# Kernel optimization log

Hardware: AMD Instinct MI355X
Metric: run time of the kernel (lower is better)

## Reference

```python
import jax, jax.numpy as jnp
import numpy as np

N_NODES = 50000
N_EDGES = 262144
N_OCP = 32768
N_GRAPHS = 64
H = 128          # hidden_size
F_IN = 128       # node feature dim (== H for the stub GNN)
N_LABELS = 10


def _lin(key, fan_in, fan_out):
    return jax.random.normal(key, (fan_in, fan_out), jnp.float32) * (1.0 / float(np.sqrt(fan_in)))


def setup_inputs() -> dict:
    key = jax.random.key(0)
    ks = jax.random.split(key, 16)
    x = jax.random.normal(ks[0], (N_NODES, F_IN), jnp.float32)
    edge_index = jax.random.randint(ks[1], (2, N_EDGES), 0, N_NODES)
    batch_vec = jnp.sort(jax.random.randint(ks[2], (N_NODES,), 0, N_GRAPHS))
    y = jax.random.randint(ks[3], (N_GRAPHS,), 0, N_LABELS)
    params = {
        # stub GNN (get_node_reps): one GCN-style layer
        'W_self': _lin(ks[4], F_IN, H),
        'W_nbr': _lin(ks[5], F_IN, H),
        'b_gnn': jnp.zeros((H,), jnp.float32),
        # edge_action_rep_generator: Linear(2H,4H) ELU Linear(4H,2H) ELU Linear(2H,H)
        'Wr1': _lin(ks[6], 2 * H, 4 * H), 'br1': jnp.zeros((4 * H,), jnp.float32),
        'Wr2': _lin(ks[7], 4 * H, 2 * H), 'br2': jnp.zeros((2 * H,), jnp.float32),
        'Wr3': _lin(ks[8], 2 * H, H),     'br3': jnp.zeros((H,), jnp.float32),
        # edge_action_prob_generator: Linear(H,H) ELU Linear(H,num_labels)
        'Wp1': _lin(ks[9], H, H),         'bp1': jnp.zeros((H,), jnp.float32),
        'Wp2': _lin(ks[10], H, N_LABELS), 'bp2': jnp.zeros((N_LABELS,), jnp.float32),
    }
    return dict(x=x, edge_index=edge_index, batch_vec=batch_vec, y=y, n_ocp=N_OCP, **params)


def reference(x, edge_index, batch_vec, y, n_ocp,
              W_self, W_nbr, b_gnn,
              Wr1, br1, Wr2, br2, Wr3, br3,
              Wp1, bp1, Wp2, bp2):
    N = x.shape[0]
    G = y.shape[0]

    def get_node_reps(ei):
        # stub for self.model.get_node_reps: elu(x @ W_self + A @ (x @ W_nbr))
        msg = x[ei[0]] @ W_nbr                                   # [E', H]
        agg = jax.ops.segment_sum(msg, ei[1], num_segments=N)    # [N, H]
        return jax.nn.elu(x @ W_self + agg + b_gnn)

    ocp_edge_index = edge_index[:, :n_ocp]    # state == True edges
    ava_edge_index = edge_index[:, n_ocp:]    # state == False edges

    ava_node_reps = get_node_reps(edge_index) - get_node_reps(ocp_edge_index)  # [N, H]

    # gather per available edge + concat src/dst reps -> [E_ava, 2H]
    a = jnp.concatenate([ava_node_reps[ava_edge_index[0]],
                         ava_node_reps[ava_edge_index[1]]], axis=1)
    # edge_action_rep_generator
    a = jax.nn.elu(a @ Wr1 + br1)
    a = jax.nn.elu(a @ Wr2 + br2)
    a = a @ Wr3 + br3                                            # [E_ava, H]
    # edge_action_prob_generator
    h = jax.nn.elu(a @ Wp1 + bp1)
    logits = h @ Wp2 + bp2                                       # [E_ava, L]

    seg = batch_vec[ava_edge_index[0]]                           # graph id per ava edge
    y_edge = y[seg]                                              # target label per edge
    sel = jnp.take_along_axis(logits, y_edge[:, None], axis=1)[:, 0]  # gather(1, y)

    # segment-wise softmax over edges of each graph
    mx = jax.ops.segment_max(sel, seg, num_segments=G)
    ex = jnp.exp(sel - mx[seg])
    probs = ex / jax.ops.segment_sum(ex, seg, num_segments=G)[seg]    # [E_ava]

    # scatter_max: per-graph max prob and its argmax edge index
    pmax = jax.ops.segment_max(probs, seg, num_segments=G)            # [G]
    E = probs.shape[0]
    idx = jnp.where(probs == pmax[seg], jnp.arange(E), E)
    added_actions = jax.ops.segment_min(idx, seg, num_segments=G)     # [G]

    return probs, pmax, added_actions
```

## Files before the change

### kernel.cpp

```cpp
#include <hip/hip_runtime.h>

#define NN   50000
#define NNP  50048
#define NE   262144
#define NOCP 32768
#define EAVA (NE - NOCP)
#define NG   64
#define HD   128
#define CAP  48
#define CHNK 32768

typedef _Float16 f16x8 __attribute__((ext_vector_type(8)));
typedef _Float16 f16x2 __attribute__((ext_vector_type(2)));
typedef float f32x4 __attribute__((ext_vector_type(4)));

#define WAITVM12() asm volatile("s_waitcnt vmcnt(12)" ::: "memory")
#define WAITVM6()  asm volatile("s_waitcnt vmcnt(6)" ::: "memory")
#define WAITVM4()  asm volatile("s_waitcnt vmcnt(4)" ::: "memory")
#define WAITVM0()  asm volatile("s_waitcnt vmcnt(0)" ::: "memory")

__device__ __forceinline__ float elu_f(float v) { return v > 0.f ? v : (expf(v) - 1.f); }

__device__ __forceinline__ unsigned fenc(float f) {
  unsigned u = __float_as_uint(f);
  return (u & 0x80000000u) ? ~u : (u | 0x80000000u);
}
__device__ __forceinline__ float fdec(unsigned u) {
  return __uint_as_float((u & 0x80000000u) ? (u & 0x7fffffffu) : ~u);
}

__device__ __forceinline__ void dma16(const void* g, void* l) {
  __builtin_amdgcn_global_load_lds((const __attribute__((address_space(1))) unsigned int*)g,
                                   (__attribute__((address_space(3))) unsigned int*)l,
                                   16, 0, 0);
}

__global__ __launch_bounds__(256) void zero_i(int* __restrict__ p, int n) {
  for (int i = blockIdx.x * 256 + threadIdx.x; i < n; i += gridDim.x * 256) p[i] = 0;
}

__global__ void init_small(unsigned* mx_enc, float* denom, unsigned* pmax_enc, int* amin) {
  int t = threadIdx.x;
  if (t < NG) { mx_enc[t] = 0u; denom[t] = 0.f; pmax_enc[t] = 0u; amin[t] = EAVA; }
}

__global__ __launch_bounds__(256) void zero_tails(_Float16* __restrict__ base) {
  int t = blockIdx.x * 256 + threadIdx.x;
  if (t >= 6 * 768) return;
  int arr = t / 768, off = t % 768;
  f16x8 z = {};
  *(f16x8*)(base + (size_t)arr * NNP * HD + (size_t)NN * HD + (size_t)off * 8) = z;
}

__global__ __launch_bounds__(256) void bucket_kernel(const int* __restrict__ ei,
    int* __restrict__ cnt, int* __restrict__ bucket) {
  int e = blockIdx.x * 256 + threadIdx.x;
  if (e >= NE) return;
  int dst = ei[NE + e];
  int src = ei[e];
  int slot = atomicAdd(&cnt[dst], 1);
  if (slot < CAP)
    bucket[(size_t)dst * CAP + slot] = (int)((unsigned)src | (e < NOCP ? 0x80000000u : 0u));
}

__global__ __launch_bounds__(256) void gather_kernel(const float* __restrict__ x,
    const int* __restrict__ cnt, const int* __restrict__ bucket,
    _Float16* __restrict__ xsah, _Float16* __restrict__ xsal,
    _Float16* __restrict__ xsoh, _Float16* __restrict__ xsol) {
  int n = blockIdx.x * 4 + (threadIdx.x >> 6);
  if (n >= NN) return;
  int lane = threadIdx.x & 63;
  int c = cnt[n];
  if (c > CAP) c = CAP;
  float2 aall = make_float2(0.f, 0.f), aocp = aall;
  const int* bk = bucket + (size_t)n * CAP;
  for (int i0 = 0; i0 < c; i0 += 4) {
    int4 pk = *(const int4*)(bk + i0);
    bool m1 = (i0 + 1 < c), m2 = (i0 + 2 < c), m3 = (i0 + 3 < c);
    int r0 = pk.x & 0x7fffffff;
    int r1 = m1 ? (pk.y & 0x7fffffff) : 0;
    int r2 = m2 ? (pk.z & 0x7fffffff) : 0;
    int r3 = m3 ? (pk.w & 0x7fffffff) : 0;
    float2 v0 = *(const float2*)(x + (size_t)r0 * HD + lane * 2);
    float2 v1 = *(const float2*)(x + (size_t)r1 * HD + lane * 2);
    float2 v2 = *(const float2*)(x + (size_t)r2 * HD + lane * 2);
    float2 v3 = *(const float2*)(x + (size_t)r3 * HD + lane * 2);
    aall.x += v0.x; aall.y += v0.y;
    if (pk.x < 0) { aocp.x += v0.x; aocp.y += v0.y; }
    if (m1) { aall.x += v1.x; aall.y += v1.y; if (pk.y < 0) { aocp.x += v1.x; aocp.y += v1.y; } }
    if (m2) { aall.x += v2.x; aall.y += v2.y; if (pk.z < 0) { aocp.x += v2.x; aocp.y += v2.y; } }
    if (m3) { aall.x += v3.x; aall.y += v3.y; if (pk.w < 0) { aocp.x += v3.x; aocp.y += v3.y; } }
  }
  size_t o = (size_t)n * HD + lane * 2;
  _Float16 h0 = (_Float16)aall.x, h1 = (_Float16)aall.y;
  *(f16x2*)(xsah + o) = (f16x2){h0, h1};
  *(f16x2*)(xsal + o) = (f16x2){(_Float16)(aall.x - (float)h0), (_Float16)(aall.y - (float)h1)};
  _Float16 g0 = (_Float16)aocp.x, g1 = (_Float16)aocp.y;
  *(f16x2*)(xsoh + o) = (f16x2){g0, g1};
  *(f16x2*)(xsol + o) = (f16x2){(_Float16)(aocp.x - (float)g0), (_Float16)(aocp.y - (float)g1)};
}

__global__ __launch_bounds__(256) void split_x(const float* __restrict__ r,
    _Float16* __restrict__ rh, _Float16* __restrict__ rl) {
  int t = blockIdx.x * 256 + threadIdx.x;
  if (t >= NN * HD / 8) return;
  const float4* p = (const float4*)(r + (size_t)t * 8);
  float4 v0 = p[0], v1 = p[1];
  float vv[8] = {v0.x, v0.y, v0.z, v0.w, v1.x, v1.y, v1.z, v1.w};
  f16x8 hv, lv;
#pragma unroll
  for (int j = 0; j < 8; ++j) {
    _Float16 hh = (_Float16)vv[j];
    hv[j] = hh;
    lv[j] = (_Float16)(vv[j] - (float)hh);
  }
  *(f16x8*)(rh + (size_t)t * 8) = hv;
  *(f16x8*)(rl + (size_t)t * 8) = lv;
}

__global__ void pack_w2(const float* __restrict__ Wself, const float* __restrict__ Wnbr,
    _Float16* __restrict__ oh, _Float16* __restrict__ ol) {
  int chunk = blockIdx.x;
  int lane = threadIdx.x;
  int ns = chunk & 7, kt = chunk >> 3;
  int n = ns * 16 + (lane & 15);
  int k0 = kt * 32 + (lane >> 4) * 8;
  f16x8 hv, lv;
#pragma unroll
  for (int j = 0; j < 8; ++j) {
    int k = k0 + j;
    float v = (k < 128) ? Wself[(size_t)k * 128 + n] : Wnbr[(size_t)(k - 128) * 128 + n];
    _Float16 hh = (_Float16)v;
    hv[j] = hh;
    lv[j] = (_Float16)(v - (float)hh);
  }
  *(f16x8*)(oh + (size_t)chunk * 512 + lane * 8) = hv;
  *(f16x8*)(ol + (size_t)chunk * 512 + lane * 8) = lv;
}

__global__ void pack_w(const float* __restrict__ W, int K, int N,
    _Float16* __restrict__ oh, _Float16* __restrict__ ol) {
  int chunk = blockIdx.x;
  int lane = threadIdx.x;
  int NS = N >> 4;
  int ns = chunk % NS, kt = chunk / NS;
  int n = ns * 16 + (lane & 15);
  int k0 = kt * 32 + (lane >> 4) * 8;
  f16x8 hv, lv;
#pragma unroll
  for (int j = 0; j < 8; ++j) {
    float v = W[(size_t)(k0 + j) * N + n];
    _Float16 hh = (_Float16)v;
    hv[j] = hh;
    lv[j] = (_Float16)(v - (float)hh);
  }
  *(f16x8*)(oh + (size_t)chunk * 512 + lane * 8) = hv;
  *(f16x8*)(ol + (size_t)chunk * 512 + lane * 8) = lv;
}

__global__ void w34_kernel(const float* __restrict__ Wr3, const float* __restrict__ Wp1,
    const float* __restrict__ br3, const float* __restrict__ bp1,
    float* __restrict__ W34, float* __restrict__ b34) {
  int i = blockIdx.x, j = threadIdx.x;
  float s = 0.f;
  for (int k = 0; k < 128; ++k) s += Wr3[i * 128 + k] * Wp1[k * 128 + j];
  W34[i * 128 + j] = s;
  if (i == 0) {
    float t = bp1[j];
    for (int k = 0; k < 128; ++k) t += br3[k] * Wp1[k * 128 + j];
    b34[j] = t;
  }
}

template <int KT, int NS_B, int AMODE, int KT_NEXT, int NB>
__global__ __launch_bounds__(256) void gemm_ab(
    const _Float16* __restrict__ Ah, const _Float16* __restrict__ Al,
    const int* __restrict__ idx0, const int* __restrict__ idx1,
    const _Float16* __restrict__ Bh, const _Float16* __restrict__ Bl,
    const float* __restrict__ bias,
    _Float16* __restrict__ Oh, _Float16* __restrict__ Ol) {
  __shared__ char smem[32768] __attribute__((aligned(16)));
  float* sC = (float*)smem;

  const int tid = threadIdx.x;
  const int w = tid >> 6, lane = tid & 63;
  const int l16 = lane & 15, g16 = lane >> 4;
  const int f = blockIdx.x;
  const int r8 = f & 7;
  const int nb = (f >> 3) % NB;
  const int q8 = f / (8 * NB);
  const int bm = (q8 * 8 + r8) * 64, bn = nb * 64;
  const int w2r = w >> 1, w2c = w & 1;
  const int bmT = bm >> 4, bnS = bn >> 4;

  f32x4 acc[2][2];
#pragma unroll
  for (int i = 0; i < 2; ++i)
#pragma unroll
    for (int j = 0; j < 2; ++j) acc[i][j] = (f32x4)0.f;

  int i0w = 0, i1w = 0;
  if constexpr (AMODE == 1) {
    int rr = bm + w * 16 + l16;
    i0w = idx0[rr];
    i1w = idx1[rr];
  }

  auto STAGE = [&](int kt, int buf) {
    char* base = smem + buf * 16384;
    if constexpr (AMODE == 0) {
      size_t ch = (size_t)(bmT + w) * KT + kt;
      dma16((const char*)Ah + ch * 1024 + lane * 16, base + w * 1024);
      dma16((const char*)Al + ch * 1024 + lane * 16, base + 4096 + w * 1024);
    } else {
      int col = (kt & 3) * 32 + g16 * 8;
      int r = (kt < 4) ? i0w : i1w;
      dma16(Ah + (size_t)r * HD + col, base + w * 1024);
      dma16(Al + (size_t)r * HD + col, base + 4096 + w * 1024);
    }
    size_t chb = (size_t)kt * NS_B + bnS + w;
    dma16((const char*)Bh + chb * 1024 + lane * 16, base + 8192 + w * 1024);
    dma16((const char*)Bl + chb * 1024 + lane * 16, base + 12288 + w * 1024);
  };

  auto COMPUTE = [&](int buf) {
    const _Float16* sAh = (const _Float16*)(smem + buf * 16384);
    const _Float16* sAl = (const _Float16*)(smem + buf * 16384 + 4096);
    const _Float16* sBh = (const _Float16*)(smem + buf * 16384 + 8192);
    const _Float16* sBl = (const _Float16*)(smem + buf * 16384 + 12288);
    f16x8 ah[2], al[2];
#pragma unroll
    for (int mi = 0; mi < 2; ++mi) {
      ah[mi] = *(const f16x8*)(sAh + (w2r * 2 + mi) * 512 + lane * 8);
      al[mi] = *(const f16x8*)(sAl + (w2r * 2 + mi) * 512 + lane * 8);
    }
#pragma unroll
    for (int ni = 0; ni < 2; ++ni) {
      f16x8 bh = *(const f16x8*)(sBh + (w2c * 2 + ni) * 512 + lane * 8);
      f16x8 bl = *(const f16x8*)(sBl + (w2c * 2 + ni) * 512 + lane * 8);
#pragma unroll
      for (int mi = 0; mi < 2; ++mi) {
        acc[mi][ni] = __builtin_amdgcn_mfma_f32_16x16x32_f16(ah[mi], bh, acc[mi][ni], 0, 0, 0);
        acc[mi][ni] = __builtin_amdgcn_mfma_f32_16x16x32_f16(al[mi], bh, acc[mi][ni], 0, 0, 0);
        acc[mi][ni] = __builtin_amdgcn_mfma_f32_16x16x32_f16(ah[mi], bl, acc[mi][ni], 0, 0, 0);
      }
    }
  };

  STAGE(0, 0);
#pragma unroll
  for (int kt = 0; kt < KT; ++kt) {
    if (kt + 1 < KT) {
      STAGE(kt + 1, (kt + 1) & 1);
      WAITVM4();
    } else {
      WAITVM0();
    }
    __builtin_amdgcn_s_barrier();
    COMPUTE(kt & 1);
    __builtin_amdgcn_s_barrier();
  }

#pragma unroll
  for (int ni = 0; ni < 2; ++ni) {
    int colL = (w2c * 2 + ni) * 16 + l16;
    float bv = bias[bn + colL];
#pragma unroll
    for (int mi = 0; mi < 2; ++mi) {
      int rowb = w2r * 32 + mi * 16 + g16 * 4;
#pragma unroll
      for (int r = 0; r < 4; ++r)
        sC[(rowb + r) * 68 + colL] = elu_f(acc[mi][ni][r] + bv);
    }
  }
  __syncthreads();
  const int bnT32 = bn >> 5;
#pragma unroll
  for (int s = 0; s < 2; ++s) {
    int chunkid = w * 2 + s;
    int msub = chunkid >> 1, ktl = chunkid & 1;
    int m = msub * 16 + l16;
    int cb = ktl * 32 + g16 * 8;
    f16x8 hv, lv;
#pragma unroll
    for (int j = 0; j < 8; ++j) {
      float v = sC[m * 68 + cb + j];
      _Float16 hh = (_Float16)v;
      hv[j] = hh;
      lv[j] = (_Float16)(v - (float)hh);
    }
    size_t gchunk = (size_t)(bmT + msub) * KT_NEXT + (bnT32 + ktl);
    *(f16x8*)((char*)Oh + gchunk * 1024 + lane * 16) = hv;
    *(f16x8*)((char*)Ol + gchunk * 1024 + lane * 16) = lv;
  }
}

__global__ __launch_bounds__(64) void reps_direct(
    const _Float16* __restrict__ xh, const _Float16* __restrict__ xl,
    const _Float16* __restrict__ xsah, const _Float16* __restrict__ xsal,
    const _Float16* __restrict__ xsoh, const _Float16* __restrict__ xsol,
    const _Float16* __restrict__ Wsh, const _Float16* __restrict__ Wsl,
    const float* __restrict__ bias,
    _Float16* __restrict__ Oh, _Float16* __restrict__ Ol) {
  __shared__ float sC[32][68];
  const int lane = threadIdx.x;
  const int mt = blockIdx.x, nt = blockIdx.y;
  const int bm = mt * 32, bn = nt * 64;
  const int l16 = lane & 15, g16 = lane >> 4;

  f32x4 acc1[2][4], acc2[2][4];
#pragma unroll
  for (int i = 0; i < 2; ++i)
#pragma unroll
    for (int j = 0; j < 4; ++j) acc1[i][j] = (f32x4)0.f;

  auto CP3 = [&](f32x4 (*acc)[4], const f16x8* ah, const f16x8* al,
                 const f16x8* bh, const f16x8* bl) {
#pragma unroll
    for (int ni = 0; ni < 4; ++ni)
#pragma unroll
      for (int mi = 0; mi < 2; ++mi) {
        acc[mi][ni] = __builtin_amdgcn_mfma_f32_16x16x32_f16(ah[mi], bh[ni], acc[mi][ni], 0, 0, 0);
        acc[mi][ni] = __builtin_amdgcn_mfma_f32_16x16x32_f16(al[mi], bh[ni], acc[mi][ni], 0, 0, 0);
        acc[mi][ni] = __builtin_amdgcn_mfma_f32_16x16x32_f16(ah[mi], bl[ni], acc[mi][ni], 0, 0, 0);
      }
  };

#pragma unroll
  for (int kt = 0; kt < 4; ++kt) {
    f16x8 ah[2], al[2], bh[4], bl[4];
#pragma unroll
    for (int mi = 0; mi < 2; ++mi) {
      size_t off = (size_t)(bm + mi * 16 + l16) * HD + kt * 32 + g16 * 8;
      ah[mi] = *(const f16x8*)(xh + off);
      al[mi] = *(const f16x8*)(xl + off);
    }
#pragma unroll
    for (int ni = 0; ni < 4; ++ni) {
      size_t ch = (size_t)kt * 8 + nt * 4 + ni;
      bh[ni] = *(const f16x8*)(Wsh + ch * 512 + lane * 8);
      bl[ni] = *(const f16x8*)(Wsl + ch * 512 + lane * 8);
    }
    CP3(acc1, ah, al, bh, bl);
  }
#pragma unroll
  for (int i = 0; i < 2; ++i)
#pragma unroll
    for (int j = 0; j < 4; ++j) acc2[i][j] = acc1[i][j];

#pragma unroll
  for (int kt = 0; kt < 4; ++kt) {
    f16x8 aah[2], aal[2], aoh[2], aol[2], bh[4], bl[4];
#pragma unroll
    for (int mi = 0; mi < 2; ++mi) {
      size_t off = (size_t)(bm + mi * 16 + l16) * HD + kt * 32 + g16 * 8;
      aah[mi] = *(const f16x8*)(xsah + off);
      aal[mi] = *(const f16x8*)(xsal + off);
      aoh[mi] = *(const f16x8*)(xsoh + off);
      aol[mi] = *(const f16x8*)(xsol + off);
    }
#pragma unroll
    for (int ni = 0; ni < 4; ++ni) {
      size_t ch = (size_t)(kt + 4) * 8 + nt * 4 + ni;
      bh[ni] = *(const f16x8*)(Wsh + ch * 512 + lane * 8);
      bl[ni] = *(const f16x8*)(Wsl + ch * 512 + lane * 8);
    }
    CP3(acc1, aah, aal, bh, bl);
    CP3(acc2, aoh, aol, bh, bl);
  }

#pragma unroll
  for (int ni = 0; ni < 4; ++ni) {
    int colL = ni * 16 + l16;
    float bv = bias[bn + colL];
#pragma unroll
    for (int mi = 0; mi < 2; ++mi) {
      int rowb = mi * 16 + g16 * 4;
#pragma unroll
      for (int r = 0; r < 4; ++r)
        sC[rowb + r][colL] = elu_f(acc1[mi][ni][r] + bv) - elu_f(acc2[mi][ni][r] + bv);
    }
  }
  __syncthreads();
#pragma unroll
  for (int c = 0; c < 4; ++c) {
    int msub = c >> 1, ktl = c & 1;
    int m = msub * 16 + l16;
    int cb = ktl * 32 + g16 * 8;
    int grow = bm + m;
    if (grow < NN) {
      f16x8 hv, lv;
#pragma unroll
      for (int j = 0; j < 8; ++j) {
        float v = sC[m][cb + j];
        _Float16 hh = (_Float16)v;
        hv[j] = hh;
        lv[j] = (_Float16)(v - (float)hh);
      }
      *(f16x8*)(Oh + (size_t)grow * HD + bn + cb) = hv;
      *(f16x8*)(Ol + (size_t)grow * HD + bn + cb) = lv;
    }
  }
}

__global__ __launch_bounds__(256) void gemm3_sel(
    const _Float16* __restrict__ Ah, const _Float16* __restrict__ Al,
    const _Float16* __restrict__ Bh, const _Float16* __restrict__ Bl,
    const float* __restrict__ b34,
    const int* __restrict__ ei, const int* __restrict__ batchv, const int* __restrict__ yv,
    const float* __restrict__ Wp2, const float* __restrict__ bp2,
    float* __restrict__ sel, int* __restrict__ seg, int co) {
  __shared__ char smem[73728] __attribute__((aligned(16)));
  const int tid = threadIdx.x;
  const int w = tid >> 6, lane = tid & 63;
  const int l16 = lane & 15, g16 = lane >> 4;
  const int mt = blockIdx.x;

  f32x4 acc[8];
#pragma unroll
  for (int j = 0; j < 8; ++j) acc[j] = (f32x4)0.f;

  auto STAGE = [&](int kt, int buf) {
    char* base = smem + buf * 24576;
    size_t ch = (size_t)(mt * 4 + w) * 8 + kt;
    dma16((const char*)Ah + ch * 1024 + lane * 16, base + w * 1024);
    dma16((const char*)Al + ch * 1024 + lane * 16, base + 4096 + w * 1024);
#pragma unroll
    for (int s = 0; s < 2; ++s) {
      int nsub = w * 2 + s;
      size_t chb = (size_t)kt * 8 + nsub;
      dma16((const char*)Bh + chb * 1024 + lane * 16, base + 8192 + nsub * 1024);
      dma16((const char*)Bl + chb * 1024 + lane * 16, base + 16384 + nsub * 1024);
    }
  };

  auto COMPUTE = [&](int buf) {
    const _Float16* sAh = (const _Float16*)(smem + buf * 24576);
    const _Float16* sAl = (const _Float16*)(smem + buf * 24576 + 4096);
    const _Float16* sBh = (const _Float16*)(smem + buf * 24576 + 8192);
    const _Float16* sBl = (const _Float16*)(smem + buf * 24576 + 16384);
    f16x8 ah = *(const f16x8*)(sAh + w * 512 + lane * 8);
    f16x8 al = *(const f16x8*)(sAl + w * 512 + lane * 8);
#pragma unroll
    for (int ni = 0; ni < 8; ++ni) {
      f16x8 bh = *(const f16x8*)(sBh + ni * 512 + lane * 8);
      f16x8 bl = *(const f16x8*)(sBl + ni * 512 + lane * 8);
      acc[ni] = __builtin_amdgcn_mfma_f32_16x16x32_f16(ah, bh, acc[ni], 0, 0, 0);
      acc[ni] = __builtin_amdgcn_mfma_f32_16x16x32_f16(al, bh, acc[ni], 0, 0, 0);
      acc[ni] = __builtin_amdgcn_mfma_f32_16x16x32_f16(ah, bl, acc[ni], 0, 0, 0);
    }
  };

  STAGE(0, 0);
  STAGE(1, 1);
#pragma unroll
  for (int kt = 0; kt < 8; ++kt) {
    if (kt + 2 < 8) STAGE(kt + 2, (kt + 2) % 3);
    if (kt < 6) WAITVM12();
    else if (kt == 6) WAITVM6();
    else WAITVM0();
    __builtin_amdgcn_s_barrier();
    COMPUTE(kt % 3);
    __builtin_amdgcn_s_barrier();
  }

  float bb[8];
#pragma unroll
  for (int ni = 0; ni < 8; ++ni) bb[ni] = b34[ni * 16 + l16];

#pragma unroll
  for (int rr = 0; rr < 4; ++rr) {
    int row = w * 16 + g16 * 4 + rr;
    int e = co + mt * 64 + row;
    int s = ei[NOCP + e];
    int gg = batchv[s];
    int c = yv[gg];
    float a = 0.f;
#pragma unroll
    for (int ni = 0; ni < 8; ++ni)
      a += elu_f(acc[ni][rr] + bb[ni]) * Wp2[(ni * 16 + l16) * 10 + c];
    a += __shfl_xor(a, 1);
    a += __shfl_xor(a, 2);
    a += __shfl_xor(a, 4);
    a += __shfl_xor(a, 8);
    if (l16 == 0) { sel[e] = a + bp2[c]; seg[e] = gg; }
  }
}

__global__ __launch_bounds__(256) void segmax_sel(const float* __restrict__ sel,
    const int* __restrict__ seg, unsigned* __restrict__ mx_enc) {
  __shared__ unsigned sm[NG];
  int tid = threadIdx.x;
  if (tid < NG) sm[tid] = 0u;
  __syncthreads();
  for (int i = blockIdx.x * blockDim.x + tid; i < EAVA; i += gridDim.x * blockDim.x)
    atomicMax(&sm[seg[i]], fenc(sel[i]));
  __syncthreads();
  if (tid < NG) atomicMax(&mx_enc[tid], sm[tid]);
}

__global__ __launch_bounds__(256) void exden_kernel(const float* __restrict__ sel,
    const int* __restrict__ seg, const unsigned* __restrict__ mx_enc,
    float* __restrict__ denom, float* __restrict__ out_probs) {
  __shared__ float sd[NG];
  __shared__ float smx[NG];
  int tid = threadIdx.x;
  if (tid < NG) { smx[tid] = fdec(mx_enc[tid]); sd[tid] = 0.f; }
  __syncthreads();
  for (int i = blockIdx.x * blockDim.x + tid; i < EAVA; i += gridDim.x * blockDim.x) {
    int g = seg[i];
    float ex = expf(sel[i] - smx[g]);
    out_probs[i] = ex;
    atomicAdd(&sd[g], ex);
  }
  __syncthreads();
  if (tid < NG) atomicAdd(&denom[tid], sd[tid]);
}

__global__ __launch_bounds__(256) void probpmax_kernel(const int* __restrict__ seg,
    const float* __restrict__ denom, float* __restrict__ out_probs,
    unsigned* __restrict__ pmax_enc) {
  __shared__ float sden[NG];
  __shared__ unsigned sp[NG];
  int tid = threadIdx.x;
  if (tid < NG) { sden[tid] = denom[tid]; sp[tid] = 0u; }
  __syncthreads();
  for (int i = blockIdx.x * blockDim.x + tid; i < EAVA; i += gridDim.x * blockDim.x) {
    int g = seg[i];
    float p = out_probs[i] / sden[g];
    out_probs[i] = p;
    atomicMax(&sp[g], fenc(p));
  }
  __syncthreads();
  if (tid < NG) atomicMax(&pmax_enc[tid], sp[tid]);
}

__global__ __launch_bounds__(256) void argmin_kernel(const int* __restrict__ seg,
    const float* __restrict__ out_probs, const unsigned* __restrict__ pmax_enc,
    int* __restrict__ amin) {
  __shared__ float spm[NG];
  __shared__ int sa[NG];
  int tid = threadIdx.x;
  if (tid < NG) { spm[tid] = fdec(pmax_enc[tid]); sa[tid] = EAVA; }
  __syncthreads();
  for (int i = blockIdx.x * blockDim.x + tid; i < EAVA; i += gridDim.x * blockDim.x) {
    int g = seg[i];
    if (out_probs[i] == spm[g]) atomicMin(&sa[g], i);
  }
  __syncthreads();
  if (tid < NG) atomicMin(&amin[tid], sa[tid]);
}

__global__ void finalize_kernel(const unsigned* __restrict__ pmax_enc,
    const int* __restrict__ amin, float* __restrict__ out) {
  int g = threadIdx.x;
  if (g < NG) {
    out[EAVA + g] = fdec(pmax_enc[g]);
    out[EAVA + NG + g] = (float)amin[g];
  }
}

extern "C" void kernel_launch(void* const* d_in, const int* in_sizes, int n_in,
                              void* d_out, int out_size, void* d_ws, size_t ws_size,
                              hipStream_t stream) {
  const float* x      = (const float*)d_in[0];
  const int*   ei     = (const int*)d_in[1];
  const int*   batchv = (const int*)d_in[2];
  const int*   yv     = (const int*)d_in[3];
  const float* Wself = (const float*)d_in[5];
  const float* Wnbr  = (const float*)d_in[6];
  const float* bgnn  = (const float*)d_in[7];
  const float* Wr1   = (const float*)d_in[8];
  const float* br1   = (const float*)d_in[9];
  const float* Wr2   = (const float*)d_in[10];
  const float* br2   = (const float*)d_in[11];
  const float* Wr3   = (const float*)d_in[12];
  const float* br3   = (const float*)d_in[13];
  const float* Wp1   = (const float*)d_in[14];
  const float* bp1   = (const float*)d_in[15];
  const float* Wp2   = (const float*)d_in[16];
  const float* bp2   = (const float*)d_in[17];
  float* out = (float*)d_out;

  char* wp = (char*)d_ws;
  auto alloc = [&](size_t bytes) -> char* {
    char* p = wp;
    wp += (bytes + 255) & ~(size_t)255;
    return p;
  };
  _Float16* xsplit = (_Float16*)alloc((size_t)6 * NNP * HD * 2);
  _Float16* xh   = xsplit + (size_t)0 * NNP * HD;
  _Float16* xl   = xsplit + (size_t)1 * NNP * HD;
  _Float16* xsah = xsplit + (size_t)2 * NNP * HD;
  _Float16* xsal = xsplit + (size_t)3 * NNP * HD;
  _Float16* xsoh = xsplit + (size_t)4 * NNP * HD;
  _Float16* xsol = xsplit + (size_t)5 * NNP * HD;
  _Float16*  reps_h   = (_Float16*)alloc((size_t)NN * HD * 2);
  _Float16*  reps_l   = (_Float16*)alloc((size_t)NN * HD * 2);
  int*       cnt      = (int*)alloc((size_t)NN * 4);
  int*       bucket   = (int*)alloc((size_t)NN * CAP * 4);
  float*     sel      = (float*)alloc((size_t)EAVA * 4);
  int*       seg      = (int*)alloc((size_t)EAVA * 4);
  unsigned*  mx_enc   = (unsigned*)alloc(NG * 4);
  float*     denom    = (float*)alloc(NG * 4);
  unsigned*  pmax_enc = (unsigned*)alloc(NG * 4);
  int*       amin     = (int*)alloc(NG * 4);
  _Float16*  Wsh  = (_Float16*)alloc((size_t)64 * 1024);
  _Float16*  Wsl  = (_Float16*)alloc((size_t)64 * 1024);
  _Float16*  Wr1h = (_Float16*)alloc((size_t)8 * 32 * 1024);
  _Float16*  Wr1l = (_Float16*)alloc((size_t)8 * 32 * 1024);
  _Float16*  Wr2h = (_Float16*)alloc((size_t)16 * 16 * 1024);
  _Float16*  Wr2l = (_Float16*)alloc((size_t)16 * 16 * 1024);
  float*     W34  = (float*)alloc((size_t)256 * 128 * 4);
  float*     b34  = (float*)alloc(128 * 4);
  _Float16*  W34h = (_Float16*)alloc((size_t)8 * 8 * 1024);
  _Float16*  W34l = (_Float16*)alloc((size_t)8 * 8 * 1024);
  _Float16*  b1h = (_Float16*)alloc((size_t)(CHNK / 16) * 16 * 1024);
  _Float16*  b1l = (_Float16*)alloc((size_t)(CHNK / 16) * 16 * 1024);
  _Float16*  b2h = (_Float16*)alloc((size_t)(CHNK / 16) * 8 * 1024);
  _Float16*  b2l = (_Float16*)alloc((size_t)(CHNK / 16) * 8 * 1024);
  (void)ws_size;

  zero_i<<<64, 256, 0, stream>>>(cnt, NN);
  init_small<<<1, 64, 0, stream>>>(mx_enc, denom, pmax_enc, amin);
  zero_tails<<<18, 256, 0, stream>>>(xsplit);
  bucket_kernel<<<NE / 256, 256, 0, stream>>>(ei, cnt, bucket);
  gather_kernel<<<(NN + 3) / 4, 256, 0, stream>>>(x, cnt, bucket, xsah, xsal, xsoh, xsol);
  split_x<<<(NN * HD / 8 + 255) / 256, 256, 0, stream>>>(x, xh, xl);
  pack_w2<<<64, 64, 0, stream>>>(Wself, Wnbr, Wsh, Wsl);
  reps_direct<<<dim3(NNP / 32, 2), 64, 0, stream>>>(xh, xl, xsah, xsal, xsoh, xsol, Wsh, Wsl,
                                                    bgnn, reps_h, reps_l);
  w34_kernel<<<256, 128, 0, stream>>>(Wr3, Wp1, br3, bp1, W34, b34);
  pack_w<<<8 * 32, 64, 0, stream>>>(Wr1, 256, 512, Wr1h, Wr1l);
  pack_w<<<16 * 16, 64, 0, stream>>>(Wr2, 512, 256, Wr2h, Wr2l);
  pack_w<<<8 * 8, 64, 0, stream>>>(W34, 256, 128, W34h, W34l);

  for (int c = 0; c < 7; ++c) {
    int co = c * CHNK;
    gemm_ab<8, 32, 1, 16, 8><<<(CHNK / 64) * 8, 256, 0, stream>>>(
        reps_h, reps_l, ei + NOCP + co, ei + NE + NOCP + co, Wr1h, Wr1l, br1, b1h, b1l);
    gemm_ab<16, 16, 0, 8, 4><<<(CHNK / 64) * 4, 256, 0, stream>>>(
        b1h, b1l, nullptr, nullptr, Wr2h, Wr2l, br2, b2h, b2l);
    gemm3_sel<<<CHNK / 64, 256, 0, stream>>>(
        b2h, b2l, W34h, W34l, b34, ei, batchv, yv, Wp2, bp2, sel, seg, co);
  }

  segmax_sel<<<112, 256, 0, stream>>>(sel, seg, mx_enc);
  exden_kernel<<<112, 256, 0, stream>>>(sel, seg, mx_enc, denom, out);
  probpmax_kernel<<<112, 256, 0, stream>>>(seg, denom, out, pmax_enc);
  argmin_kernel<<<112, 256, 0, stream>>>(seg, out, pmax_enc, amin);
  finalize_kernel<<<1, 64, 0, stream>>>(pmax_enc, amin, out);
}
```

Before: 931.6 us.

## Interleave hi/lo node reps per row and add swizzled gather GEMM1 kernel

Stores the fp16 hi and lo halves of node representations interleaved in a single 256-element row per node, so the first MLP GEMM's gathered rows are fetched as contiguous 128-byte segments rather than from two separate arrays. A dedicated gemm1_il kernel loads each gathered row with per-lane 16-byte DMAs into an XOR-swizzled LDS layout to avoid bank conflicts, and the generic gemm_ab drops its gather mode. The aim is better coalescing and fewer scattered memory transactions in the gather-heavy first GEMM. The cost is a more complex, specialised kernel and a different LDS read pattern.

Measured after the change: 826.0 us (median of 2 runs). 11.3% less time.

```diff
diff --git a/kernel.cpp b/kernel.cpp
--- a/kernel.cpp
+++ b/kernel.cpp
@@ -172,9 +172,9 @@
   }
 }
 
-template <int KT, int NS_B, int AMODE, int KT_NEXT, int NB>
-__global__ __launch_bounds__(256) void gemm_ab(
-    const _Float16* __restrict__ Ah, const _Float16* __restrict__ Al,
+template <int NB>
+__global__ __launch_bounds__(256) void gemm1_il(
+    const _Float16* __restrict__ Rhl,
     const int* __restrict__ idx0, const int* __restrict__ idx1,
     const _Float16* __restrict__ Bh, const _Float16* __restrict__ Bl,
     const float* __restrict__ bias,
@@ -199,25 +199,131 @@
 #pragma unroll
     for (int j = 0; j < 2; ++j) acc[i][j] = (f32x4)0.f;
 
-  int i0w = 0, i1w = 0;
-  if constexpr (AMODE == 1) {
-    int rr = bm + w * 16 + l16;
-    i0w = idx0[rr];
-    i1w = idx1[rr];
-  }
+  const int rl = lane >> 3, t8 = lane & 7;
+  const int sub = t8 ^ (rl & 7);
+  const int i0a = idx0[bm + w * 16 + rl];
+  const int i0b = idx0[bm + w * 16 + 8 + rl];
+  const int i1a = idx1[bm + w * 16 + rl];
+  const int i1b = idx1[bm + w * 16 + 8 + rl];
 
   auto STAGE = [&](int kt, int buf) {
     char* base = smem + buf * 16384;
-    if constexpr (AMODE == 0) {
-      size_t ch = (size_t)(bmT + w) * KT + kt;
-      dma16((const char*)Ah + ch * 1024 + lane * 16, base + w * 1024);
-      dma16((const char*)Al + ch * 1024 + lane * 16, base + 4096 + w * 1024);
+    int ktb = kt & 3;
+#pragma unroll
+    for (int s = 0; s < 2; ++s) {
+      int r = (kt < 4) ? (s == 0 ? i0a : i0b) : (s == 0 ? i1a : i1b);
+      dma16(Rhl + (size_t)r * 256 + ktb * 64 + sub * 8,
+            base + w * 2048 + s * 1024 + lane * 16);
+    }
+    size_t chb = (size_t)kt * 32 + bnS + w;
+    dma16((const char*)Bh + chb * 1024 + lane * 16, base + 8192 + w * 1024);
+    dma16((const char*)Bl + chb * 1024 + lane * 16, base + 12288 + w * 1024);
+  };
+
+  auto COMPUTE = [&](int buf) {
+    const _Float16* sA = (const _Float16*)(smem + buf * 16384);
+    const _Float16* sBh = (const _Float16*)(smem + buf * 16384 + 8192);
+    const _Float16* sBl = (const _Float16*)(smem + buf * 16384 + 12288);
+    const int sw = l16 & 7;
+    f16x8 ah[2], al[2];
+#pragma unroll
+    for (int mi = 0; mi < 2; ++mi) {
+      const _Float16* mb = sA + (w2r * 2 + mi) * 1024 + l16 * 64;
+      ah[mi] = *(const f16x8*)(mb + (g16 ^ sw) * 8);
+      al[mi] = *(const f16x8*)(mb + ((g16 + 4) ^ sw) * 8);
+    }
+#pragma unroll
+    for (int ni = 0; ni < 2; ++ni) {
+      f16x8 bh = *(const f16x8*)(sBh + (w2c * 2 + ni) * 512 + lane * 8);
+      f16x8 bl = *(const f16x8*)(sBl + (w2c * 2 + ni) * 512 + lane * 8);
+#pragma unroll
+      for (int mi = 0; mi < 2; ++mi) {
+        acc[mi][ni] = __builtin_amdgcn_mfma_f32_16x16x32_f16(ah[mi], bh, acc[mi][ni], 0, 0, 0);
+        acc[mi][ni] = __builtin_amdgcn_mfma_f32_16x16x32_f16(al[mi], bh, acc[mi][ni], 0, 0, 0);
+        acc[mi][ni] = __builtin_amdgcn_mfma_f32_16x16x32_f16(ah[mi], bl, acc[mi][ni], 0, 0, 0);
+      }
+    }
+  };
+
+  STAGE(0, 0);
+#pragma unroll
+  for (int kt = 0; kt < 8; ++kt) {
+    if (kt + 1 < 8) {
+      STAGE(kt + 1, (kt + 1) & 1);
+      WAITVM4();
     } else {
-      int col = (kt & 3) * 32 + g16 * 8;
-      int r = (kt < 4) ? i0w : i1w;
-      dma16(Ah + (size_t)r * HD + col, base + w * 1024);
-      dma16(Al + (size_t)r * HD + col, base + 4096 + w * 1024);
-    }
+      WAITVM0();
+    }
+    __builtin_amdgcn_s_barrier();
+    COMPUTE(kt & 1);
+    __builtin_amdgcn_s_barrier();
+  }
+
+#pragma unroll
+  for (int ni = 0; ni < 2; ++ni) {
+    int colL = (w2c * 2 + ni) * 16 + l16;
+    float bv = bias[bn + colL];
+#pragma unroll
+    for (int mi = 0; mi < 2; ++mi) {
+      int rowb = w2r * 32 + mi * 16 + g16 * 4;
+#pragma unroll
+      for (int r = 0; r < 4; ++r)
+        sC[(rowb + r) * 68 + colL] = elu_f(acc[mi][ni][r] + bv);
+    }
+  }
+  __syncthreads();
+  const int bnT32 = bn >> 5;
+#pragma unroll
+  for (int s = 0; s < 2; ++s) {
+    int chunkid = w * 2 + s;
+    int msub = chunkid >> 1, ktl = chunkid & 1;
+    int m = msub * 16 + l16;
+    int cb = ktl * 32 + g16 * 8;
+    f16x8 hv, lv;
+#pragma unroll
+    for (int j = 0; j < 8; ++j) {
+      float v = sC[m * 68 + cb + j];
+      _Float16 hh = (_Float16)v;
+      hv[j] = hh;
+      lv[j] = (_Float16)(v - (float)hh);
+    }
+    size_t gchunk = (size_t)(bmT + msub) * 16 + (bnT32 + ktl);
+    *(f16x8*)((char*)Oh + gchunk * 1024 + lane * 16) = hv;
+    *(f16x8*)((char*)Ol + gchunk * 1024 + lane * 16) = lv;
+  }
+}
+
+template <int KT, int NS_B, int KT_NEXT, int NB>
+__global__ __launch_bounds__(256) void gemm_ab(
+    const _Float16* __restrict__ Ah, const _Float16* __restrict__ Al,
+    const _Float16* __restrict__ Bh, const _Float16* __restrict__ Bl,
+    const float* __restrict__ bias,
+    _Float16* __restrict__ Oh, _Float16* __restrict__ Ol) {
+  __shared__ char smem[32768] __attribute__((aligned(16)));
+  float* sC = (float*)smem;
+
+  const int tid = threadIdx.x;
+  const int w = tid >> 6, lane = tid & 63;
+  const int l16 = lane & 15, g16 = lane >> 4;
+  const int f = blockIdx.x;
+  const int r8 = f & 7;
+  const int nb = (f >> 3) % NB;
+  const int q8 = f / (8 * NB);
+  const int bm = (q8 * 8 + r8) * 64, bn = nb * 64;
+  const int w2r = w >> 1, w2c = w & 1;
+  const int bmT = bm >> 4, bnS = bn >> 4;
+
+  f32x4 acc[2][2];
+#pragma unroll
+  for (int i = 0; i < 2; ++i)
+#pragma unroll
+    for (int j = 0; j < 2; ++j) acc[i][j] = (f32x4)0.f;
+
+  auto STAGE = [&](int kt, int buf) {
+    char* base = smem + buf * 16384;
+    size_t ch = (size_t)(bmT + w) * KT + kt;
+    dma16((const char*)Ah + ch * 1024 + lane * 16, base + w * 1024);
+    dma16((const char*)Al + ch * 1024 + lane * 16, base + 4096 + w * 1024);
     size_t chb = (size_t)kt * NS_B + bnS + w;
     dma16((const char*)Bh + chb * 1024 + lane * 16, base + 8192 + w * 1024);
     dma16((const char*)Bl + chb * 1024 + lane * 16, base + 12288 + w * 1024);
@@ -301,7 +407,7 @@
     const _Float16* __restrict__ xsoh, const _Float16* __restrict__ xsol,
     const _Float16* __restrict__ Wsh, const _Float16* __restrict__ Wsl,
     const float* __restrict__ bias,
-    _Float16* __restrict__ Oh, _Float16* __restrict__ Ol) {
+    _Float16* __restrict__ Rhl) {
   __shared__ float sC[32][68];
   const int lane = threadIdx.x;
   const int mt = blockIdx.x, nt = blockIdx.y;
@@ -397,8 +503,10 @@
         hv[j] = hh;
         lv[j] = (_Float16)(v - (float)hh);
       }
-      *(f16x8*)(Oh + (size_t)grow * HD + bn + cb) = hv;
-      *(f16x8*)(Ol + (size_t)grow * HD + bn + cb) = lv;
+      int ktg = (bn >> 5) + ktl;
+      size_t o = (size_t)grow * 256 + ktg * 64 + g16 * 8;
+      *(f16x8*)(Rhl + o) = hv;
+      *(f16x8*)(Rhl + o + 32) = lv;
     }
   }
 }
@@ -595,8 +703,7 @@
   _Float16* xsal = xsplit + (size_t)3 * NNP * HD;
   _Float16* xsoh = xsplit + (size_t)4 * NNP * HD;
   _Float16* xsol = xsplit + (size_t)5 * NNP * HD;
-  _Float16*  reps_h   = (_Float16*)alloc((size_t)NN * HD * 2);
-  _Float16*  reps_l   = (_Float16*)alloc((size_t)NN * HD * 2);
+  _Float16*  reps_hl  = (_Float16*)alloc((size_t)NN * 256 * 2);
   int*       cnt      = (int*)alloc((size_t)NN * 4);
   int*       bucket   = (int*)alloc((size_t)NN * CAP * 4);
   float*     sel      = (float*)alloc((size_t)EAVA * 4);
@@ -629,7 +736,7 @@
   split_x<<<(NN * HD / 8 + 255) / 256, 256, 0, stream>>>(x, xh, xl);
   pack_w2<<<64, 64, 0, stream>>>(Wself, Wnbr, Wsh, Wsl);
   reps_direct<<<dim3(NNP / 32, 2), 64, 0, stream>>>(xh, xl, xsah, xsal, xsoh, xsol, Wsh, Wsl,
-                                                    bgnn, reps_h, reps_l);
+                                                    bgnn, reps_hl);
   w34_kernel<<<256, 128, 0, stream>>>(Wr3, Wp1, br3, bp1, W34, b34);
   pack_w<<<8 * 32, 64, 0, stream>>>(Wr1, 256, 512, Wr1h, Wr1l);
   pack_w<<<16 * 16, 64, 0, stream>>>(Wr2, 512, 256, Wr2h, Wr2l);
@@ -637,10 +744,10 @@
 
   for (int c = 0; c < 7; ++c) {
     int co = c * CHNK;
-    gemm_ab<8, 32, 1, 16, 8><<<(CHNK / 64) * 8, 256, 0, stream>>>(
-        reps_h, reps_l, ei + NOCP + co, ei + NE + NOCP + co, Wr1h, Wr1l, br1, b1h, b1l);
-    gemm_ab<16, 16, 0, 8, 4><<<(CHNK / 64) * 4, 256, 0, stream>>>(
-        b1h, b1l, nullptr, nullptr, Wr2h, Wr2l, br2, b2h, b2l);
+    gemm1_il<8><<<(CHNK / 64) * 8, 256, 0, stream>>>(
+        reps_hl, ei + NOCP + co, ei + NE + NOCP + co, Wr1h, Wr1l, br1, b1h, b1l);
+    gemm_ab<16, 16, 8, 4><<<(CHNK / 64) * 4, 256, 0, stream>>>(
+        b1h, b1l, Wr2h, Wr2l, br2, b2h, b2l);
     gemm3_sel<<<CHNK / 64, 256, 0, stream>>>(
         b2h, b2l, W34h, W34l, b34, ei, batchv, yv, Wp2, bp2, sel, seg, co);
   }
```
